# Kernel tuning notes

Measured on AMD Instinct MI355X. Metric: run time of the kernel, lower is better.

## Reference

```python
import jax, jax.numpy as jnp
import numpy as np

N_E = 50000
N_R = 1000
E = 800000
E_HIDDEN = 256
R_HIDDEN = 64
NEG_SLOPE = 0.01  # torch F.leaky_relu default


def segment_softmax(logits, seg, num_segments):
    # numerically stable per-segment softmax over edges
    seg_max = jax.ops.segment_max(logits, seg, num_segments=num_segments)
    seg_max = jnp.where(jnp.isfinite(seg_max), seg_max, 0.0)
    ex = jnp.exp(logits - seg_max[seg])
    denom = jax.ops.segment_sum(ex, seg, num_segments=num_segments)
    return ex / (denom[seg] + 1e-16)


def setup_inputs() -> dict:
    key = jax.random.key(0)
    ks = jax.random.split(key, 9)
    return {
        "x_e": jax.random.normal(ks[0], (N_E, E_HIDDEN), dtype=jnp.float32),
        "x_r": jax.random.normal(ks[1], (N_R, R_HIDDEN), dtype=jnp.float32),
        "edge_index": jax.random.randint(ks[2], (2, E), 0, N_E, dtype=jnp.int64),
        "rel": jax.random.randint(ks[3], (E,), 0, N_R, dtype=jnp.int64),
        "line_graph_index": jax.random.randint(ks[4], (2, E), 0, E, dtype=jnp.int64),
        "line_graph_val": jax.random.uniform(ks[5], (E,), dtype=jnp.float32),
        "a_h_w": jax.random.normal(ks[6], (E_HIDDEN,), dtype=jnp.float32),
        "a_t_w": jax.random.normal(ks[7], (E_HIDDEN,), dtype=jnp.float32),
        "a_r_w": jax.random.normal(ks[8], (R_HIDDEN,), dtype=jnp.float32),
    }


def reference(x_e, x_r, edge_index, rel, line_graph_index, line_graph_val, a_h_w, a_t_w, a_r_w):
    head, tail = edge_index[0], edge_index[1]
    # per-node scalar scores, gathered per edge
    s_e_h = jnp.einsum("nd,d->n", x_e, a_h_w)  # [N_e]
    s_e_t = jnp.einsum("nd,d->n", x_e, a_t_w)  # [N_e]
    s_r = jnp.einsum("rd,d->r", x_r, a_r_w)    # [N_r]
    e_h = s_e_h[head]
    e_t = s_e_t[tail]
    e_r = s_r[rel]

    n_e = x_e.shape[0]
    msg = x_r[rel]  # [E, r_hidden]

    # head branch: segment softmax over head groups, scatter-aggregate x_r[rel]
    alpha_h = segment_softmax(jax.nn.leaky_relu(e_h + e_r, NEG_SLOPE), head, n_e)
    x_e_h = jax.ops.segment_sum(alpha_h[:, None] * msg, head, num_segments=n_e)

    # tail branch: softmax grouped by tail, but spmm still scatters into head rows
    alpha_t = segment_softmax(jax.nn.leaky_relu(e_t + e_r, NEG_SLOPE), tail, n_e)
    x_e_t = jax.ops.segment_sum(alpha_t[:, None] * msg, tail, num_segments=n_e)

    return jnp.concatenate([x_e_h, x_e_t], axis=1)  # [N_e, 2*r_hidden]
```

## Files before the change

### kernel.cpp

```cpp
#include <hip/hip_runtime.h>

static constexpr int kNE = 50000;
static constexpr int kNR = 1000;
static constexpr int kE  = 800000;
static constexpr int kEH = 256;
static constexpr int kRH = 64;
static constexpr float kNeg = 0.01f;

static constexpr int kSegsPerB = 64;
static constexpr int kSegs = 2 * kNE;
static constexpr int kB = (kSegs + kSegsPerB - 1) / kSegsPerB;
static constexpr int kCap = 1536;
static constexpr int kEdgesPerBin = 4096;
static constexpr int kBinBlocks  = (kE + kEdgesPerBin - 1) / kEdgesPerBin;
static constexpr int kNodeBlocks = kNE / 8;
static constexpr int kRelBlocks  = kNR / 8;
static constexpr int kCntPad = 2048;

__device__ __forceinline__ float lrelu(float x){ return x > 0.f ? x : kNeg * x; }

__global__ __launch_bounds__(512) void k_bin_scores(
        const float* __restrict__ xe, const float* __restrict__ ahw,
        const float* __restrict__ atw, const float* __restrict__ xr,
        const float* __restrict__ arw,
        const int* __restrict__ head, const int* __restrict__ tail,
        const int* __restrict__ rel,
        float* __restrict__ s_h, float* __restrict__ s_t, float* __restrict__ s_r,
        int* __restrict__ bucket_fill, unsigned short* __restrict__ records){
    __shared__ int cnt[kCntPad];
    __shared__ int cur[kCntPad];
    __shared__ unsigned int srt[2 * kEdgesPerBin];
    __shared__ int wsum[8];

    int blk = blockIdx.x;
    int tid = threadIdx.x;
    int lane = tid & 63;

    if (blk >= kBinBlocks){
        int sb = blk - kBinBlocks;
        if (sb < kNodeBlocks){
            int node = sb * 8 + (tid >> 6);
            const float4* row = (const float4*)(xe + (size_t)node * kEH);
            float4 xv = row[lane];
            float4 av = ((const float4*)ahw)[lane];
            float4 bv = ((const float4*)atw)[lane];
            float ph = xv.x*av.x + xv.y*av.y + xv.z*av.z + xv.w*av.w;
            float pt = xv.x*bv.x + xv.y*bv.y + xv.z*bv.z + xv.w*bv.w;
            #pragma unroll
            for (int o = 32; o > 0; o >>= 1){
                ph += __shfl_down(ph, o, 64);
                pt += __shfl_down(pt, o, 64);
            }
            if (lane == 0){ s_h[node] = ph; s_t[node] = pt; }
        } else {
            int r = (sb - kNodeBlocks) * 8 + (tid >> 6);
            float p = xr[(size_t)r * kRH + lane] * arw[lane];
            #pragma unroll
            for (int o = 32; o > 0; o >>= 1) p += __shfl_down(p, o, 64);
            if (lane == 0) s_r[r] = p;
        }
        return;
    }

    int e0 = blk * kEdgesPerBin;
    for (int i = tid; i < kCntPad; i += 512) cnt[i] = 0;
    __syncthreads();

    unsigned int recs[16];
    #pragma unroll
    for (int p = 0; p < 8; ++p){
        int e = e0 + p * 512 + tid;
        unsigned int rh = 0xFFFFFFFFu, rt = 0xFFFFFFFFu;
        if (e < kE){
            int h = head[e], t = tail[e], r = rel[e];
            rh = ((unsigned int)h << 10) | (unsigned int)r;
            rt = ((unsigned int)(kNE + t) << 10) | (unsigned int)r;
            atomicAdd(&cnt[rh >> 16], 1);
            atomicAdd(&cnt[rt >> 16], 1);
        }
        recs[p] = rh; recs[8 + p] = rt;
    }
    __syncthreads();

    int c0 = cnt[4 * tid], c1 = cnt[4 * tid + 1], c2 = cnt[4 * tid + 2], c3 = cnt[4 * tid + 3];
    int v = c0 + c1 + c2 + c3;
    int x = v;
    #pragma unroll
    for (int o = 1; o < 64; o <<= 1){
        int y = __shfl_up(x, o, 64);
        if (lane >= o) x += y;
    }
    int wv = tid >> 6;
    if (lane == 63) wsum[wv] = x;
    __syncthreads();
    int wpre = 0, tot = 0;
    #pragma unroll
    for (int w = 0; w < 8; ++w){
        int s = wsum[w];
        if (w < wv) wpre += s;
        tot += s;
    }
    int base = wpre + x - v;
    cur[4 * tid]     = base;
    cur[4 * tid + 1] = base + c0;
    cur[4 * tid + 2] = base + c0 + c1;
    cur[4 * tid + 3] = base + c0 + c1 + c2;
    __syncthreads();

    #pragma unroll
    for (int p = 0; p < 16; ++p){
        unsigned int rc = recs[p];
        if (rc != 0xFFFFFFFFu){
            int slot = atomicAdd(&cur[rc >> 16], 1);
            srt[slot] = rc;
        }
    }
    __syncthreads();

    for (int i = tid; i < kB; i += 512){
        int c = cnt[i];
        if (c > 0){
            int gb = atomicAdd(&bucket_fill[i], c);
            cur[i] = gb - (cur[i] - c);
        }
    }
    __syncthreads();

    for (int j = tid; j < tot; j += 512){
        unsigned int rc = srt[j];
        int bk = rc >> 16;
        int g  = cur[bk] + j;
        if (g < kCap) records[(size_t)bk * kCap + g] = (unsigned short)(rc & 0xFFFFu);
    }
}

__global__ __launch_bounds__(256) void k_sort_aggregate(
        const int* __restrict__ bucket_fill, const unsigned short* __restrict__ records,
        const float* __restrict__ s_h, const float* __restrict__ s_t,
        const float* __restrict__ s_r, const float* __restrict__ xr,
        float* __restrict__ out){
    __shared__ float srl[kNR];
    __shared__ float sn[kSegsPerB];
    __shared__ unsigned short relbuf[kCap];
    __shared__ float alphabuf[kCap];
    __shared__ int cnt[kSegsPerB], start[kSegsPerB], cur[kSegsPerB];

    int b = blockIdx.x;
    int tid = threadIdx.x;

    for (int i = tid; i < kNR; i += 256) srl[i] = s_r[i];
    if (tid < kSegsPerB){
        cnt[tid] = 0;
        int gseg = b * kSegsPerB + tid;
        float s = 0.f;
        if (gseg < kNE) s = s_h[gseg];
        else if (gseg < kSegs) s = s_t[gseg - kNE];
        sn[tid] = s;
    }
    __syncthreads();

    int nrec = bucket_fill[b];
    if (nrec > kCap) nrec = kCap;
    const unsigned short* rb = records + (size_t)b * kCap;

    unsigned short recs[6];
    #pragma unroll
    for (int p = 0; p < 6; ++p){
        int idx = p * 256 + tid;
        unsigned short rc = 0xFFFFu;
        if (idx < nrec){
            rc = rb[idx];
            atomicAdd(&cnt[rc >> 10], 1);
        }
        recs[p] = rc;
    }
    __syncthreads();
    if (tid < kSegsPerB){
        int c = cnt[tid];
        int x = c;
        #pragma unroll
        for (int o = 1; o < 64; o <<= 1){
            int y = __shfl_up(x, o, 64);
            if (tid >= o) x += y;
        }
        int s = x - c;
        start[tid] = s;
        cur[tid] = s;
    }
    __syncthreads();
    #pragma unroll
    for (int p = 0; p < 6; ++p){
        unsigned short rc = recs[p];
        if (rc != 0xFFFFu){
            int ls = rc >> 10;
            int rr = rc & 1023;
            int slot = atomicAdd(&cur[ls], 1);
            relbuf[slot] = (unsigned short)rr;
            alphabuf[slot] = lrelu(sn[ls] + srl[rr]);
        }
    }
    __syncthreads();

    int grp = tid >> 4;
    int sub = tid & 15;
    for (int ls = grp; ls < kSegsPerB; ls += 16){
        int gseg = b * kSegsPerB + ls;
        if (gseg >= kSegs) break;
        int deg = cnt[ls], st = start[ls];

        float part = -INFINITY;
        for (int k = sub; k < deg; k += 16) part = fmaxf(part, alphabuf[st + k]);
        #pragma unroll
        for (int o = 1; o < 16; o <<= 1) part = fmaxf(part, __shfl_xor(part, o, 64));
        float m = part;

        float ss = 0.f;
        for (int k = sub; k < deg; k += 16){
            float e = __expf(alphabuf[st + k] - m);
            alphabuf[st + k] = e;
            ss += e;
        }
        #pragma unroll
        for (int o = 1; o < 16; o <<= 1) ss += __shfl_xor(ss, o, 64);
        float inv = 1.f / (ss + 1e-16f);

        float4 acc = {0.f, 0.f, 0.f, 0.f};
        int k = 0;
        for (; k + 4 <= deg; k += 4){
            int r0 = relbuf[st + k],     r1 = relbuf[st + k + 1];
            int r2 = relbuf[st + k + 2], r3 = relbuf[st + k + 3];
            float a0 = alphabuf[st + k] * inv,     a1 = alphabuf[st + k + 1] * inv;
            float a2 = alphabuf[st + k + 2] * inv, a3 = alphabuf[st + k + 3] * inv;
            float4 v0 = ((const float4*)(xr + (size_t)r0 * kRH))[sub];
            float4 v1 = ((const float4*)(xr + (size_t)r1 * kRH))[sub];
            float4 v2 = ((const float4*)(xr + (size_t)r2 * kRH))[sub];
            float4 v3 = ((const float4*)(xr + (size_t)r3 * kRH))[sub];
            acc.x += a0*v0.x + a1*v1.x + a2*v2.x + a3*v3.x;
            acc.y += a0*v0.y + a1*v1.y + a2*v2.y + a3*v3.y;
            acc.z += a0*v0.z + a1*v1.z + a2*v2.z + a3*v3.z;
            acc.w += a0*v0.w + a1*v1.w + a2*v2.w + a3*v3.w;
        }
        for (; k < deg; ++k){
            int rr = relbuf[st + k];
            float a = alphabuf[st + k] * inv;
            float4 v = ((const float4*)(xr + (size_t)rr * kRH))[sub];
            acc.x += a*v.x; acc.y += a*v.y; acc.z += a*v.z; acc.w += a*v.w;
        }
        bool isHead = gseg < kNE;
        int node = isHead ? gseg : gseg - kNE;
        float4* op = (float4*)(out + (size_t)node * (2 * kRH) + (isHead ? 0 : kRH));
        op[sub] = acc;
    }
}

extern "C" void kernel_launch(void* const* d_in, const int* in_sizes, int n_in,
                              void* d_out, int out_size, void* d_ws, size_t ws_size,
                              hipStream_t stream) {
    const float* xe  = (const float*)d_in[0];
    const float* xr  = (const float*)d_in[1];
    const int* edge_index = (const int*)d_in[2];
    const int* rel        = (const int*)d_in[3];
    const float* ahw = (const float*)d_in[6];
    const float* atw = (const float*)d_in[7];
    const float* arw = (const float*)d_in[8];
    float* out = (float*)d_out;

    const int* head = edge_index;
    const int* tail = edge_index + kE;

    char* ws = (char*)d_ws;
    float* s_h  = (float*)ws;                    ws += kNE * sizeof(float);
    float* s_t  = (float*)ws;                    ws += kNE * sizeof(float);
    float* s_r  = (float*)ws;                    ws += kNR * sizeof(float);
    int*   bucket_fill = (int*)ws;               ws += ((kB + 255) & ~255) * sizeof(int);
    unsigned short* records = (unsigned short*)ws; ws += (size_t)kB * kCap * sizeof(unsigned short);

    hipMemsetAsync(bucket_fill, 0, kB * sizeof(int), stream);
    k_bin_scores<<<kBinBlocks + kNodeBlocks + kRelBlocks, 512, 0, stream>>>(
        xe, ahw, atw, xr, arw, head, tail, rel, s_h, s_t, s_r, bucket_fill, records);
    k_sort_aggregate<<<kB, 256, 0, stream>>>(bucket_fill, records, s_h, s_t, s_r, xr, out);
}
```

Baseline: 158.7 us.

## Reuse counting-atomic ranks for scatter, degree-sort segments, defer softmax normalization

Both kernels now keep the return value of the counting atomicAdd as each record's rank, so the scatter phase computes its slot as start+rank instead of issuing a second shared-memory atomic. The aggregate kernel bitonic-sorts its 64 segments by degree within one wavefront so the 16-thread groups handle segments of similar length, reducing imbalance across a group's four iterations. The softmax normalization is applied once to the accumulator instead of to every alpha. The global offset update changes to match, since cur is no longer advanced. The cost is extra registers for the ranks and a short shuffle sort.

```diff
diff --git a/kernel.cpp b/kernel.cpp
--- a/kernel.cpp
+++ b/kernel.cpp
@@ -67,18 +67,21 @@
     __syncthreads();
 
     unsigned int recs[16];
+    unsigned short rnk[16];
     #pragma unroll
     for (int p = 0; p < 8; ++p){
         int e = e0 + p * 512 + tid;
         unsigned int rh = 0xFFFFFFFFu, rt = 0xFFFFFFFFu;
+        unsigned short kh = 0, kt = 0;
         if (e < kE){
             int h = head[e], t = tail[e], r = rel[e];
             rh = ((unsigned int)h << 10) | (unsigned int)r;
             rt = ((unsigned int)(kNE + t) << 10) | (unsigned int)r;
-            atomicAdd(&cnt[rh >> 16], 1);
-            atomicAdd(&cnt[rt >> 16], 1);
+            kh = (unsigned short)atomicAdd(&cnt[rh >> 16], 1);
+            kt = (unsigned short)atomicAdd(&cnt[rt >> 16], 1);
         }
         recs[p] = rh; recs[8 + p] = rt;
+        rnk[p]  = kh; rnk[8 + p]  = kt;
     }
     __syncthreads();
 
@@ -111,7 +114,7 @@
     for (int p = 0; p < 16; ++p){
         unsigned int rc = recs[p];
         if (rc != 0xFFFFFFFFu){
-            int slot = atomicAdd(&cur[rc >> 16], 1);
+            int slot = cur[rc >> 16] + (int)rnk[p];
             srt[slot] = rc;
         }
     }
@@ -121,7 +124,7 @@
         int c = cnt[i];
         if (c > 0){
             int gb = atomicAdd(&bucket_fill[i], c);
-            cur[i] = gb - (cur[i] - c);
+            cur[i] = gb - cur[i];
         }
     }
     __syncthreads();
@@ -143,7 +146,8 @@
     __shared__ float sn[kSegsPerB];
     __shared__ unsigned short relbuf[kCap];
     __shared__ float alphabuf[kCap];
-    __shared__ int cnt[kSegsPerB], start[kSegsPerB], cur[kSegsPerB];
+    __shared__ int cnt[kSegsPerB], start[kSegsPerB];
+    __shared__ unsigned short order[kSegsPerB];
 
     int b = blockIdx.x;
     int tid = threadIdx.x;
@@ -163,16 +167,16 @@
     if (nrec > kCap) nrec = kCap;
     const unsigned short* rb = records + (size_t)b * kCap;
 
-    unsigned short recs[6];
+    unsigned short recs[6], rnk[6];
     #pragma unroll
     for (int p = 0; p < 6; ++p){
         int idx = p * 256 + tid;
-        unsigned short rc = 0xFFFFu;
+        unsigned short rc = 0xFFFFu, rk = 0;
         if (idx < nrec){
             rc = rb[idx];
-            atomicAdd(&cnt[rc >> 10], 1);
-        }
-        recs[p] = rc;
+            rk = (unsigned short)atomicAdd(&cnt[rc >> 10], 1);
+        }
+        recs[p] = rc; rnk[p] = rk;
     }
     __syncthreads();
     if (tid < kSegsPerB){
@@ -183,9 +187,21 @@
             int y = __shfl_up(x, o, 64);
             if (tid >= o) x += y;
         }
-        int s = x - c;
-        start[tid] = s;
-        cur[tid] = s;
+        start[tid] = x - c;
+
+        unsigned int key = ((unsigned int)c << 6) | (unsigned int)tid;
+        #pragma unroll
+        for (int k = 2; k <= 64; k <<= 1){
+            #pragma unroll
+            for (int j = k >> 1; j > 0; j >>= 1){
+                unsigned int o2 = __shfl_xor(key, j, 64);
+                bool keepMin = (((tid & j) == 0) == ((tid & k) == 0));
+                unsigned int mn = key < o2 ? key : o2;
+                unsigned int mx = key < o2 ? o2 : key;
+                key = keepMin ? mn : mx;
+            }
+        }
+        order[tid] = (unsigned short)(key & 63u);
     }
     __syncthreads();
     #pragma unroll
@@ -194,7 +210,7 @@
         if (rc != 0xFFFFu){
             int ls = rc >> 10;
             int rr = rc & 1023;
-            int slot = atomicAdd(&cur[ls], 1);
+            int slot = start[ls] + (int)rnk[p];
             relbuf[slot] = (unsigned short)rr;
             alphabuf[slot] = lrelu(sn[ls] + srl[rr]);
         }
@@ -203,9 +219,11 @@
 
     int grp = tid >> 4;
     int sub = tid & 15;
-    for (int ls = grp; ls < kSegsPerB; ls += 16){
+    #pragma unroll
+    for (int i = 0; i < 4; ++i){
+        int ls = order[i * 16 + grp];
         int gseg = b * kSegsPerB + ls;
-        if (gseg >= kSegs) break;
+        if (gseg >= kSegs) continue;
         int deg = cnt[ls], st = start[ls];
 
         float part = -INFINITY;
@@ -229,8 +247,8 @@
         for (; k + 4 <= deg; k += 4){
             int r0 = relbuf[st + k],     r1 = relbuf[st + k + 1];
             int r2 = relbuf[st + k + 2], r3 = relbuf[st + k + 3];
-            float a0 = alphabuf[st + k] * inv,     a1 = alphabuf[st + k + 1] * inv;
-            float a2 = alphabuf[st + k + 2] * inv, a3 = alphabuf[st + k + 3] * inv;
+            float a0 = alphabuf[st + k],     a1 = alphabuf[st + k + 1];
+            float a2 = alphabuf[st + k + 2], a3 = alphabuf[st + k + 3];
             float4 v0 = ((const float4*)(xr + (size_t)r0 * kRH))[sub];
             float4 v1 = ((const float4*)(xr + (size_t)r1 * kRH))[sub];
             float4 v2 = ((const float4*)(xr + (size_t)r2 * kRH))[sub];
@@ -242,10 +260,12 @@
         }
         for (; k < deg; ++k){
             int rr = relbuf[st + k];
-            float a = alphabuf[st + k] * inv;
+            float a = alphabuf[st + k];
             float4 v = ((const float4*)(xr + (size_t)rr * kRH))[sub];
             acc.x += a*v.x; acc.y += a*v.y; acc.z += a*v.z; acc.w += a*v.w;
         }
+        acc.x *= inv; acc.y *= inv; acc.z *= inv; acc.w *= inv;
+
         bool isHead = gseg < kNE;
         int node = isHead ? gseg : gseg - kNE;
         float4* op = (float4*)(out + (size_t)node * (2 * kRH) + (isHead ? 0 : kRH));
```

Result: no change. 155.9 us (-1.8%).
